# Optimization experiments

Hardware: AMD Instinct MI355X
Metric: run time of the kernel (lower is better)

Reference implementation:

```python
import jax, jax.numpy as jnp
import numpy as np

L2_REG = 0.02
EPS = 1e-8  # torch F.cosine_similarity eps


def setup_inputs() -> dict:
    key = jax.random.key(0)
    N, d = 8192, 512
    examples = jax.random.normal(key, (N, 2, d), dtype=jnp.float32)
    return {"examples": examples}


def reference(examples):
    # examples: (N, 2, d)
    anchors = examples[:, 0, :]    # (N, d)
    positives = examples[:, 1, :]  # (N, d)

    a_norm = jnp.linalg.norm(anchors, axis=-1)    # (N,)
    p_norm = jnp.linalg.norm(positives, axis=-1)  # (N,)

    # positive similarity: cos(a_i, p_i), torch-style eps clamp on norm product
    pos_sim = jnp.sum(anchors * positives, axis=-1) / jnp.maximum(a_norm * p_norm, EPS)  # (N,)

    # full cosine similarity matrix S[i, j] = cos(a_i, p_j) via normalized GEMM
    dots = jnp.einsum('id,jd->ij', anchors, positives)  # (N, N)
    denom = jnp.maximum(a_norm[:, None] * p_norm[None, :], EPS)
    neg_sim = dots / denom

    # diagonal of negatives is replaced by the anchor itself: cos(a_i, a_i)
    diag_val = (a_norm * a_norm) / jnp.maximum(a_norm * a_norm, EPS)  # ~1.0, eps-faithful
    N = anchors.shape[0]
    idx = jnp.arange(N)
    neg_sim = neg_sim.at[idx, idx].set(diag_val)

    logits = jnp.concatenate([pos_sim[:, None], neg_sim], axis=1)  # (N, N+1)
    # cross-entropy with labels all zero -> -log_softmax(...)[:, 0], mean over N
    ce = -jnp.mean(jax.nn.log_softmax(logits, axis=-1)[:, 0])

    l2_term = L2_REG * jnp.linalg.norm(examples)  # Frobenius norm of full input
    return ce + l2_term
```

## Files before the change

### kernel.cpp

```cpp
#include <hip/hip_runtime.h>
#include <hip/hip_bf16.h>


#define NR 8192
#define DD 512
#define E_CONST 2.71828182845904523536f

typedef __attribute__((ext_vector_type(8))) short bf16x8_t;
typedef __attribute__((ext_vector_type(4))) float f32x4_t;

__device__ __forceinline__ ushort f2bf(float x) {
    __hip_bfloat16 h = __float2bfloat16(x);
    return *reinterpret_cast<ushort*>(&h);
}

__global__ __launch_bounds__(128) void prep_kernel(
    const float* __restrict__ ex,
    ushort* __restrict__ Ah, ushort* __restrict__ Ph,
    float* __restrict__ pos_sim, float* __restrict__ norm2,
    float* __restrict__ rowsum, float* __restrict__ part)
{
    const int i = blockIdx.x;
    const int t = threadIdx.x;
    const float4 a = ((const float4*)(ex + (size_t)i * 1024))[t];
    const float4 p = ((const float4*)(ex + (size_t)i * 1024 + 512))[t];
    float sa  = a.x*a.x + a.y*a.y + a.z*a.z + a.w*a.w;
    float sp  = p.x*p.x + p.y*p.y + p.z*p.z + p.w*p.w;
    float sap = a.x*p.x + a.y*p.y + a.z*p.z + a.w*p.w;
    #pragma unroll
    for (int m = 1; m < 64; m <<= 1) {
        sa  += __shfl_xor(sa,  m, 64);
        sp  += __shfl_xor(sp,  m, 64);
        sap += __shfl_xor(sap, m, 64);
    }
    __shared__ float red[3][2];
    if ((t & 63) == 0) { red[0][t>>6] = sa; red[1][t>>6] = sp; red[2][t>>6] = sap; }
    __syncthreads();
    sa  = red[0][0] + red[0][1];
    sp  = red[1][0] + red[1][1];
    sap = red[2][0] + red[2][1];
    const float inva = rsqrtf(sa);
    const float invp = rsqrtf(sp);
    ushort4 av, pv;
    av.x = f2bf(a.x * inva); av.y = f2bf(a.y * inva);
    av.z = f2bf(a.z * inva); av.w = f2bf(a.w * inva);
    pv.x = f2bf(p.x * invp); pv.y = f2bf(p.y * invp);
    pv.z = f2bf(p.z * invp); pv.w = f2bf(p.w * invp);
    ((ushort4*)(Ah + (size_t)i * DD))[t] = av;
    ((ushort4*)(Ph + (size_t)i * DD))[t] = pv;
    if (t == 0) {
        pos_sim[i] = sap * inva * invp;
        norm2[i]   = sa + sp;
        rowsum[i]  = 0.0f;
        if (i == 0) { part[0] = 0.0f; part[1] = 0.0f; }
    }
}

__global__ __launch_bounds__(512, 2) void gemm_kernel(
    const ushort* __restrict__ Ah, const ushort* __restrict__ Ph,
    float* __restrict__ rowsum)
{
    __shared__ ushort ls[65536];
    const int t  = threadIdx.x;
    const int w  = t >> 6;
    const int l  = t & 63;
    const int wr = w >> 2, wc = w & 3;
    const int ll = l & 15, lh = l >> 4;
    const int m0 = blockIdx.y * 256;
    const int n0 = blockIdx.x * 256;

    f32x4_t acc[8][4];
    #pragma unroll
    for (int i = 0; i < 8; i++)
        #pragma unroll
        for (int j = 0; j < 4; j++)
            acc[i][j] = (f32x4_t){0.f, 0.f, 0.f, 0.f};

    const int srow  = t >> 3;
    const int gslot = (t & 7) ^ (srow & 7);

    auto stage = [&](int buf, int kt) {
        #pragma unroll
        for (int j = 0; j < 4; ++j) {
            const int row = j * 64 + srow;
            const char* ga = (const char*)Ah + (size_t)(m0 + row) * (DD * 2)
                             + kt * 128 + gslot * 16;
            const char* gb = (const char*)Ph + (size_t)(n0 + row) * (DD * 2)
                             + kt * 128 + gslot * 16;
            __builtin_amdgcn_global_load_lds(
                (const __attribute__((address_space(1))) void*)ga,
                (__attribute__((address_space(3))) void*)&ls[buf * 32768 + j * 4096 + t * 8],
                16, 0, 0);
            __builtin_amdgcn_global_load_lds(
                (const __attribute__((address_space(1))) void*)gb,
                (__attribute__((address_space(3))) void*)&ls[buf * 32768 + 16384 + j * 4096 + t * 8],
                16, 0, 0);
        }
    };

    auto compute = [&](int buf) {
        const int aB = buf * 32768;
        const int bB = buf * 32768 + 16384;
        #pragma unroll
        for (int ks = 0; ks < 2; ++ks) {
            bf16x8_t af[8], bfv[4];
            #pragma unroll
            for (int mi = 0; mi < 8; ++mi) {
                const int R  = wr * 128 + mi * 16 + ll;
                const int ss = (ks * 4 + lh) ^ (R & 7);
                af[mi] = *(const bf16x8_t*)&ls[aB + R * 64 + ss * 8];
            }
            #pragma unroll
            for (int ni = 0; ni < 4; ++ni) {
                const int R  = wc * 64 + ni * 16 + ll;
                const int ss = (ks * 4 + lh) ^ (R & 7);
                bfv[ni] = *(const bf16x8_t*)&ls[bB + R * 64 + ss * 8];
            }
            __builtin_amdgcn_s_setprio(1);
            #pragma unroll
            for (int mi = 0; mi < 8; ++mi)
                #pragma unroll
                for (int ni = 0; ni < 4; ++ni)
                    acc[mi][ni] = __builtin_amdgcn_mfma_f32_16x16x32_bf16(
                        af[mi], bfv[ni], acc[mi][ni], 0, 0, 0);
            __builtin_amdgcn_s_setprio(0);
        }
    };

    stage(0, 0);
    __syncthreads();
    int cur = 0;
    #pragma unroll 1
    for (int kt = 0; kt < (DD / 64) - 1; ++kt) {
        stage(cur ^ 1, kt + 1);
        compute(cur);
        __syncthreads();
        cur ^= 1;
    }
    compute(cur);

    #pragma unroll
    for (int mi = 0; mi < 8; ++mi) {
        #pragma unroll
        for (int r = 0; r < 4; ++r) {
            float s = __expf(acc[mi][0][r]) + __expf(acc[mi][1][r]) +
                      __expf(acc[mi][2][r]) + __expf(acc[mi][3][r]);
            s += __shfl_xor(s, 1, 64);
            s += __shfl_xor(s, 2, 64);
            s += __shfl_xor(s, 4, 64);
            s += __shfl_xor(s, 8, 64);
            if (ll == 0)
                atomicAdd(&rowsum[m0 + wr * 128 + mi * 16 + lh * 4 + r], s);
        }
    }
}

__global__ __launch_bounds__(256) void final1_kernel(
    const float* __restrict__ rowsum, const float* __restrict__ pos_sim,
    const float* __restrict__ norm2, float* __restrict__ part)
{
    const int i = blockIdx.x * 256 + threadIdx.x;
    float s1 = logf(rowsum[i] + E_CONST) - pos_sim[i];
    float s2 = norm2[i];
    #pragma unroll
    for (int m = 1; m < 64; m <<= 1) {
        s1 += __shfl_xor(s1, m, 64);
        s2 += __shfl_xor(s2, m, 64);
    }
    if ((threadIdx.x & 63) == 0) {
        atomicAdd(&part[0], s1);
        atomicAdd(&part[1], s2);
    }
}

__global__ void final2_kernel(const float* __restrict__ part, float* __restrict__ out)
{
    out[0] = part[0] * (1.0f / NR) + 0.02f * sqrtf(part[1]);
}

extern "C" void kernel_launch(void* const* d_in, const int* in_sizes, int n_in,
                              void* d_out, int out_size, void* d_ws, size_t ws_size,
                              hipStream_t stream) {
    const float* ex = (const float*)d_in[0];
    float* out = (float*)d_out;
    char* ws = (char*)d_ws;
    ushort* Ah     = (ushort*)(ws);
    ushort* Ph     = (ushort*)(ws + 8388608);
    float*  possim = (float*)(ws + 16777216);
    float*  norm2  = (float*)(ws + 16777216 + 32768);
    float*  rowsum = (float*)(ws + 16777216 + 65536);
    float*  part   = (float*)(ws + 16777216 + 98304);

    prep_kernel<<<NR, 128, 0, stream>>>(ex, Ah, Ph, possim, norm2, rowsum, part);
    gemm_kernel<<<dim3(NR / 256, NR / 256), 512, 0, stream>>>(Ah, Ph, rowsum);
    final1_kernel<<<NR / 256, 256, 0, stream>>>(rowsum, possim, norm2, part);
    final2_kernel<<<1, 1, 0, stream>>>(part, out);
}
```

Before: 207.1 us.

## Triple-buffer GEMM with K=32 stages, split A/B loads, and XCD-aware block remap

Restructures the bf16 GEMM main loop into a three-stage LDS ring with 32-wide K slices, issuing A and B prefetches in separate halves interleaved with MFMA bursts. Explicit vmcnt/lgkmcnt waits and barriers replace the single __syncthreads per step. A 1D grid with a block-id remap groups tiles per XCD to improve L2 locality. LDS drops to 96KB, but the loop now has more barriers per K step and uses a new swizzle pattern.

```diff
diff --git a/kernel.cpp b/kernel.cpp
--- a/kernel.cpp
+++ b/kernel.cpp
@@ -8,6 +8,8 @@
 
 typedef __attribute__((ext_vector_type(8))) short bf16x8_t;
 typedef __attribute__((ext_vector_type(4))) float f32x4_t;
+#define AS1 __attribute__((address_space(1)))
+#define AS3 __attribute__((address_space(3)))
 
 __device__ __forceinline__ ushort f2bf(float x) {
     __hip_bfloat16 h = __float2bfloat16(x);
@@ -60,14 +62,16 @@
     const ushort* __restrict__ Ah, const ushort* __restrict__ Ph,
     float* __restrict__ rowsum)
 {
-    __shared__ ushort ls[65536];
+    __shared__ ushort ls[49152];
     const int t  = threadIdx.x;
     const int w  = t >> 6;
     const int l  = t & 63;
     const int wr = w >> 2, wc = w & 3;
     const int ll = l & 15, lh = l >> 4;
-    const int m0 = blockIdx.y * 256;
-    const int n0 = blockIdx.x * 256;
+
+    const int wgid = (blockIdx.x & 7) * 128 + (blockIdx.x >> 3);
+    const int m0 = (wgid >> 5) * 256;
+    const int n0 = (wgid & 31) * 256;
 
     f32x4_t acc[8][4];
     #pragma unroll
@@ -76,68 +80,86 @@
         for (int j = 0; j < 4; j++)
             acc[i][j] = (f32x4_t){0.f, 0.f, 0.f, 0.f};
 
-    const int srow  = t >> 3;
-    const int gslot = (t & 7) ^ (srow & 7);
-
-    auto stage = [&](int buf, int kt) {
-        #pragma unroll
-        for (int j = 0; j < 4; ++j) {
-            const int row = j * 64 + srow;
-            const char* ga = (const char*)Ah + (size_t)(m0 + row) * (DD * 2)
-                             + kt * 128 + gslot * 16;
-            const char* gb = (const char*)Ph + (size_t)(n0 + row) * (DD * 2)
-                             + kt * 128 + gslot * 16;
+    auto stage = [&](int buf, int kt, const ushort* src, int chunkOff, int rowBase) {
+        #pragma unroll
+        for (int j = 0; j < 2; ++j) {
+            const int r   = w * 32 + j * 16 + (l >> 2);
+            const int gsl = (l & 3) ^ ((r >> 1) & 3);
+            const char* g = (const char*)src + (size_t)(rowBase + r) * (DD * 2)
+                            + kt * 64 + gsl * 16;
             __builtin_amdgcn_global_load_lds(
-                (const __attribute__((address_space(1))) void*)ga,
-                (__attribute__((address_space(3))) void*)&ls[buf * 32768 + j * 4096 + t * 8],
-                16, 0, 0);
-            __builtin_amdgcn_global_load_lds(
-                (const __attribute__((address_space(1))) void*)gb,
-                (__attribute__((address_space(3))) void*)&ls[buf * 32768 + 16384 + j * 4096 + t * 8],
+                (const AS1 void*)g,
+                (AS3 void*)((char*)ls + buf * 32768 + chunkOff
+                            + w * 2048 + j * 1024 + l * 16),
                 16, 0, 0);
         }
     };
 
-    auto compute = [&](int buf) {
-        const int aB = buf * 32768;
-        const int bB = buf * 32768 + 16384;
-        #pragma unroll
-        for (int ks = 0; ks < 2; ++ks) {
-            bf16x8_t af[8], bfv[4];
+    const int sA = lh ^ ((ll >> 1) & 3);
+
+    stage(0, 0, Ah, 0,     m0);
+    stage(0, 0, Ph, 16384, n0);
+    stage(1, 1, Ah, 0,     m0);
+    stage(1, 1, Ph, 16384, n0);
+    asm volatile("s_waitcnt vmcnt(4)" ::: "memory");
+    __builtin_amdgcn_s_barrier();
+    __builtin_amdgcn_sched_barrier(0);
+
+    int bufc = 0, bufn = 2;
+    #pragma unroll 1
+    for (int kt = 0; kt < DD / 32; ++kt) {
+        const int aB = bufc * 16384;
+        const int bB = bufc * 16384 + 8192;
+
+        bf16x8_t a0[4], bfv[4];
+        #pragma unroll
+        for (int mi = 0; mi < 4; ++mi)
+            a0[mi] = *(const bf16x8_t*)&ls[aB + (wr * 128 + mi * 16 + ll) * 32 + sA * 8];
+        #pragma unroll
+        for (int ni = 0; ni < 4; ++ni)
+            bfv[ni] = *(const bf16x8_t*)&ls[bB + (wc * 64 + ni * 16 + ll) * 32 + sA * 8];
+        if (kt < DD / 32 - 2) stage(bufn, kt + 2, Ah, 0, m0);
+        __builtin_amdgcn_s_barrier();
+        asm volatile("s_waitcnt lgkmcnt(0)" ::: "memory");
+        __builtin_amdgcn_sched_barrier(0);
+        __builtin_amdgcn_s_setprio(1);
+        #pragma unroll
+        for (int mi = 0; mi < 4; ++mi)
             #pragma unroll
-            for (int mi = 0; mi < 8; ++mi) {
-                const int R  = wr * 128 + mi * 16 + ll;
-                const int ss = (ks * 4 + lh) ^ (R & 7);
-                af[mi] = *(const bf16x8_t*)&ls[aB + R * 64 + ss * 8];
-            }
+            for (int ni = 0; ni < 4; ++ni)
+                acc[mi][ni] = __builtin_amdgcn_mfma_f32_16x16x32_bf16(
+                    a0[mi], bfv[ni], acc[mi][ni], 0, 0, 0);
+        __builtin_amdgcn_s_setprio(0);
+        __builtin_amdgcn_s_barrier();
+
+        bf16x8_t a1[4];
+        #pragma unroll
+        for (int mi = 0; mi < 4; ++mi)
+            a1[mi] = *(const bf16x8_t*)&ls[aB + (wr * 128 + (mi + 4) * 16 + ll) * 32 + sA * 8];
+        if (kt < DD / 32 - 2) stage(bufn, kt + 2, Ph, 16384, n0);
+        __builtin_amdgcn_s_barrier();
+        asm volatile("s_waitcnt lgkmcnt(0)" ::: "memory");
+        __builtin_amdgcn_sched_barrier(0);
+        __builtin_amdgcn_s_setprio(1);
+        #pragma unroll
+        for (int mi = 0; mi < 4; ++mi)
             #pragma unroll
-            for (int ni = 0; ni < 4; ++ni) {
-                const int R  = wc * 64 + ni * 16 + ll;
-                const int ss = (ks * 4 + lh) ^ (R & 7);
-                bfv[ni] = *(const bf16x8_t*)&ls[bB + R * 64 + ss * 8];
-            }
-            __builtin_amdgcn_s_setprio(1);
-            #pragma unroll
-            for (int mi = 0; mi < 8; ++mi)
-                #pragma unroll
-                for (int ni = 0; ni < 4; ++ni)
-                    acc[mi][ni] = __builtin_amdgcn_mfma_f32_16x16x32_bf16(
-                        af[mi], bfv[ni], acc[mi][ni], 0, 0, 0);
-            __builtin_amdgcn_s_setprio(0);
+            for (int ni = 0; ni < 4; ++ni)
+                acc[mi + 4][ni] = __builtin_amdgcn_mfma_f32_16x16x32_bf16(
+                    a1[mi], bfv[ni], acc[mi + 4][ni], 0, 0, 0);
+        __builtin_amdgcn_s_setprio(0);
+
+        if (kt < DD / 32 - 2) {
+            asm volatile("s_waitcnt vmcnt(4)" ::: "memory");
+        } else {
+            asm volatile("s_waitcnt vmcnt(0)" ::: "memory");
         }
-    };
-
-    stage(0, 0);
-    __syncthreads();
-    int cur = 0;
-    #pragma unroll 1
-    for (int kt = 0; kt < (DD / 64) - 1; ++kt) {
-        stage(cur ^ 1, kt + 1);
-        compute(cur);
-        __syncthreads();
-        cur ^= 1;
-    }
-    compute(cur);
+        __builtin_amdgcn_s_barrier();
+        __builtin_amdgcn_sched_barrier(0);
+
+        bufc = (bufc == 2) ? 0 : bufc + 1;
+        bufn = (bufn == 2) ? 0 : bufn + 1;
+    }
 
     #pragma unroll
     for (int mi = 0; mi < 8; ++mi) {
@@ -192,7 +214,7 @@
     float*  part   = (float*)(ws + 16777216 + 98304);
 
     prep_kernel<<<NR, 128, 0, stream>>>(ex, Ah, Ph, possim, norm2, rowsum, part);
-    gemm_kernel<<<dim3(NR / 256, NR / 256), 512, 0, stream>>>(Ah, Ph, rowsum);
+    gemm_kernel<<<(NR / 256) * (NR / 256), 512, 0, stream>>>(Ah, Ph, rowsum);
     final1_kernel<<<NR / 256, 256, 0, stream>>>(rowsum, possim, norm2, part);
     final2_kernel<<<1, 1, 0, stream>>>(part, out);
 }
```

New measurement: 250.8 us. 21.1% more time.

## Switch normalized GEMM operands to FP8 with scaled MFMA and merge final kernels

Applied to the files above, without the earlier changes.

Normalized anchors and positives are now quantized to FP8 (e4m3) instead of bf16, and the similarity GEMM uses the MFMA scale 16x16x128 f8f6f4 instruction with unit scales. This halves operand bytes and LDS traffic, cuts the k-loop to 4 stages of 128, and doubles the per-instruction MFMA throughput. The two final reduction kernels are merged into one single-block kernel, which drops a launch and the atomics. The risk is lower precision in the logits feeding exp and log, which could shift the loss beyond tolerance.

```diff
diff --git a/kernel.cpp b/kernel.cpp
--- a/kernel.cpp
+++ b/kernel.cpp
@@ -6,19 +6,19 @@
 #define DD 512
 #define E_CONST 2.71828182845904523536f
 
-typedef __attribute__((ext_vector_type(8))) short bf16x8_t;
 typedef __attribute__((ext_vector_type(4))) float f32x4_t;
-
-__device__ __forceinline__ ushort f2bf(float x) {
-    __hip_bfloat16 h = __float2bfloat16(x);
-    return *reinterpret_cast<ushort*>(&h);
-}
+typedef __attribute__((ext_vector_type(4))) int   i32x4_t;
+typedef __attribute__((ext_vector_type(8))) int   i32x8_t;
+typedef unsigned char uchar;
+typedef unsigned int  uint;
+#define AS1 __attribute__((address_space(1)))
+#define AS3 __attribute__((address_space(3)))
 
 __global__ __launch_bounds__(128) void prep_kernel(
     const float* __restrict__ ex,
-    ushort* __restrict__ Ah, ushort* __restrict__ Ph,
+    uchar* __restrict__ Ah, uchar* __restrict__ Ph,
     float* __restrict__ pos_sim, float* __restrict__ norm2,
-    float* __restrict__ rowsum, float* __restrict__ part)
+    float* __restrict__ rowsum)
 {
     const int i = blockIdx.x;
     const int t = threadIdx.x;
@@ -41,26 +41,25 @@
     sap = red[2][0] + red[2][1];
     const float inva = rsqrtf(sa);
     const float invp = rsqrtf(sp);
-    ushort4 av, pv;
-    av.x = f2bf(a.x * inva); av.y = f2bf(a.y * inva);
-    av.z = f2bf(a.z * inva); av.w = f2bf(a.w * inva);
-    pv.x = f2bf(p.x * invp); pv.y = f2bf(p.y * invp);
-    pv.z = f2bf(p.z * invp); pv.w = f2bf(p.w * invp);
-    ((ushort4*)(Ah + (size_t)i * DD))[t] = av;
-    ((ushort4*)(Ph + (size_t)i * DD))[t] = pv;
+    uint pa = 0, pp = 0;
+    pa = __builtin_amdgcn_cvt_pk_fp8_f32(a.x * inva, a.y * inva, pa, false);
+    pa = __builtin_amdgcn_cvt_pk_fp8_f32(a.z * inva, a.w * inva, pa, true);
+    pp = __builtin_amdgcn_cvt_pk_fp8_f32(p.x * invp, p.y * invp, pp, false);
+    pp = __builtin_amdgcn_cvt_pk_fp8_f32(p.z * invp, p.w * invp, pp, true);
+    ((uint*)Ah)[i * 128 + t] = pa;
+    ((uint*)Ph)[i * 128 + t] = pp;
     if (t == 0) {
         pos_sim[i] = sap * inva * invp;
         norm2[i]   = sa + sp;
         rowsum[i]  = 0.0f;
-        if (i == 0) { part[0] = 0.0f; part[1] = 0.0f; }
     }
 }
 
 __global__ __launch_bounds__(512, 2) void gemm_kernel(
-    const ushort* __restrict__ Ah, const ushort* __restrict__ Ph,
+    const uchar* __restrict__ Ah, const uchar* __restrict__ Ph,
     float* __restrict__ rowsum)
 {
-    __shared__ ushort ls[65536];
+    __shared__ uchar ls[131072];
     const int t  = threadIdx.x;
     const int w  = t >> 6;
     const int l  = t & 63;
@@ -76,68 +75,66 @@
         for (int j = 0; j < 4; j++)
             acc[i][j] = (f32x4_t){0.f, 0.f, 0.f, 0.f};
 
-    const int srow  = t >> 3;
-    const int gslot = (t & 7) ^ (srow & 7);
-
-    auto stage = [&](int buf, int kt) {
+    auto stage = [&](const uchar* src, int s, int matOff, int rowBase) {
+        const int buf = s & 1;
         #pragma unroll
         for (int j = 0; j < 4; ++j) {
-            const int row = j * 64 + srow;
-            const char* ga = (const char*)Ah + (size_t)(m0 + row) * (DD * 2)
-                             + kt * 128 + gslot * 16;
-            const char* gb = (const char*)Ph + (size_t)(n0 + row) * (DD * 2)
-                             + kt * 128 + gslot * 16;
+            const int r  = w * 32 + j * 8 + (l >> 3);
+            const int gs = (l & 7) ^ (r & 7);
+            const uchar* g = src + (size_t)(rowBase + r) * DD + s * 128 + gs * 16;
             __builtin_amdgcn_global_load_lds(
-                (const __attribute__((address_space(1))) void*)ga,
-                (__attribute__((address_space(3))) void*)&ls[buf * 32768 + j * 4096 + t * 8],
-                16, 0, 0);
-            __builtin_amdgcn_global_load_lds(
-                (const __attribute__((address_space(1))) void*)gb,
-                (__attribute__((address_space(3))) void*)&ls[buf * 32768 + 16384 + j * 4096 + t * 8],
+                (const AS1 void*)g,
+                (AS3 void*)(&ls[buf * 65536 + matOff + w * 4096 + j * 1024 + l * 16]),
                 16, 0, 0);
         }
     };
 
-    auto compute = [&](int buf) {
-        const int aB = buf * 32768;
-        const int bB = buf * 32768 + 16384;
+    auto rdfrag = [&](int base, int R) -> i32x8_t {
+        const int rb = base + R * 128;
+        i32x4_t lo = *(const i32x4_t*)&ls[rb + (((lh * 2)    ) ^ (ll & 7)) * 16];
+        i32x4_t hi = *(const i32x4_t*)&ls[rb + (((lh * 2) + 1) ^ (ll & 7)) * 16];
+        return __builtin_shufflevector(lo, hi, 0, 1, 2, 3, 4, 5, 6, 7);
+    };
+
+    stage(Ah, 0, 0,     m0);
+    stage(Ph, 0, 32768, n0);
+    __syncthreads();
+
+    #pragma unroll
+    for (int s = 0; s < 4; ++s) {
+        if (s < 3) {
+            stage(Ah, s + 1, 0,     m0);
+            stage(Ph, s + 1, 32768, n0);
+        }
+        const int aB = (s & 1) * 65536;
+        const int bB = aB + 32768;
+
+        i32x8_t bf[4];
         #pragma unroll
-        for (int ks = 0; ks < 2; ++ks) {
-            bf16x8_t af[8], bfv[4];
+        for (int ni = 0; ni < 4; ++ni)
+            bf[ni] = rdfrag(bB, wc * 64 + ni * 16 + ll);
+
+        #pragma unroll
+        for (int mih = 0; mih < 2; ++mih) {
+            i32x8_t af[4];
             #pragma unroll
-            for (int mi = 0; mi < 8; ++mi) {
-                const int R  = wr * 128 + mi * 16 + ll;
-                const int ss = (ks * 4 + lh) ^ (R & 7);
-                af[mi] = *(const bf16x8_t*)&ls[aB + R * 64 + ss * 8];
-            }
-            #pragma unroll
-            for (int ni = 0; ni < 4; ++ni) {
-                const int R  = wc * 64 + ni * 16 + ll;
-                const int ss = (ks * 4 + lh) ^ (R & 7);
-                bfv[ni] = *(const bf16x8_t*)&ls[bB + R * 64 + ss * 8];
-            }
+            for (int mi2 = 0; mi2 < 4; ++mi2)
+                af[mi2] = rdfrag(aB, wr * 128 + (mih * 4 + mi2) * 16 + ll);
             __builtin_amdgcn_s_setprio(1);
             #pragma unroll
-            for (int mi = 0; mi < 8; ++mi)
+            for (int mi2 = 0; mi2 < 4; ++mi2)
                 #pragma unroll
                 for (int ni = 0; ni < 4; ++ni)
-                    acc[mi][ni] = __builtin_amdgcn_mfma_f32_16x16x32_bf16(
-                        af[mi], bfv[ni], acc[mi][ni], 0, 0, 0);
+                    acc[mih * 4 + mi2][ni] =
+                        __builtin_amdgcn_mfma_scale_f32_16x16x128_f8f6f4(
+                            af[mi2], bf[ni], acc[mih * 4 + mi2][ni],
+                            0, 0,
+                            0, 0x7F7F7F7F,
+                            0, 0x7F7F7F7F);
             __builtin_amdgcn_s_setprio(0);
         }
-    };
-
-    stage(0, 0);
-    __syncthreads();
-    int cur = 0;
-    #pragma unroll 1
-    for (int kt = 0; kt < (DD / 64) - 1; ++kt) {
-        stage(cur ^ 1, kt + 1);
-        compute(cur);
         __syncthreads();
-        cur ^= 1;
     }
-    compute(cur);
 
     #pragma unroll
     for (int mi = 0; mi < 8; ++mi) {
@@ -155,27 +152,32 @@
     }
 }
 
-__global__ __launch_bounds__(256) void final1_kernel(
+__global__ __launch_bounds__(1024) void final_kernel(
     const float* __restrict__ rowsum, const float* __restrict__ pos_sim,
-    const float* __restrict__ norm2, float* __restrict__ part)
+    const float* __restrict__ norm2, float* __restrict__ out)
 {
-    const int i = blockIdx.x * 256 + threadIdx.x;
-    float s1 = logf(rowsum[i] + E_CONST) - pos_sim[i];
-    float s2 = norm2[i];
+    const int t = threadIdx.x;
+    float s1 = 0.f, s2 = 0.f;
+    #pragma unroll
+    for (int k = 0; k < NR / 1024; ++k) {
+        const int i = k * 1024 + t;
+        s1 += logf(rowsum[i] + E_CONST) - pos_sim[i];
+        s2 += norm2[i];
+    }
     #pragma unroll
     for (int m = 1; m < 64; m <<= 1) {
         s1 += __shfl_xor(s1, m, 64);
         s2 += __shfl_xor(s2, m, 64);
     }
-    if ((threadIdx.x & 63) == 0) {
-        atomicAdd(&part[0], s1);
-        atomicAdd(&part[1], s2);
+    __shared__ float r1[16], r2[16];
+    if ((t & 63) == 0) { r1[t >> 6] = s1; r2[t >> 6] = s2; }
+    __syncthreads();
+    if (t == 0) {
+        float a = 0.f, b = 0.f;
+        #pragma unroll
+        for (int k = 0; k < 16; ++k) { a += r1[k]; b += r2[k]; }
+        out[0] = a * (1.0f / NR) + 0.02f * sqrtf(b);
     }
-}
-
-__global__ void final2_kernel(const float* __restrict__ part, float* __restrict__ out)
-{
-    out[0] = part[0] * (1.0f / NR) + 0.02f * sqrtf(part[1]);
 }
 
 extern "C" void kernel_launch(void* const* d_in, const int* in_sizes, int n_in,
@@ -184,15 +186,13 @@
     const float* ex = (const float*)d_in[0];
     float* out = (float*)d_out;
     char* ws = (char*)d_ws;
-    ushort* Ah     = (ushort*)(ws);
-    ushort* Ph     = (ushort*)(ws + 8388608);
-    float*  possim = (float*)(ws + 16777216);
-    float*  norm2  = (float*)(ws + 16777216 + 32768);
-    float*  rowsum = (float*)(ws + 16777216 + 65536);
-    float*  part   = (float*)(ws + 16777216 + 98304);
+    uchar* Ah      = (uchar*)(ws);
+    uchar* Ph      = (uchar*)(ws + 4194304);
+    float* possim  = (float*)(ws + 8388608);
+    float* norm2   = (float*)(ws + 8388608 + 32768);
+    float* rowsum  = (float*)(ws + 8388608 + 65536);
 
-    prep_kernel<<<NR, 128, 0, stream>>>(ex, Ah, Ph, possim, norm2, rowsum, part);
+    prep_kernel<<<NR, 128, 0, stream>>>(ex, Ah, Ph, possim, norm2, rowsum);
     gemm_kernel<<<dim3(NR / 256, NR / 256), 512, 0, stream>>>(Ah, Ph, rowsum);
-    final1_kernel<<<NR / 256, 256, 0, stream>>>(rowsum, possim, norm2, part);
-    final2_kernel<<<1, 1, 0, stream>>>(part, out);
+    final_kernel<<<1, 1024, 0, stream>>>(rowsum, possim, norm2, out);
 }
```

After: 213.5 us. +3.1%, slower.
